# Optimization experiments

Measured on AMD Instinct MI355X. Metric: run time of the kernel, lower is better.

Reference implementation:

```python
import jax, jax.numpy as jnp
import numpy as np

DT = 0.001   # time step (s)
DX = 10.0    # grid spacing (m)


def setup_inputs() -> dict:
    key = jax.random.key(0)
    k1, k2, k3, k4, k5, k6 = jax.random.split(key, 6)
    B, H, W, NT, NR = 2, 256, 256, 600, 128
    # source wavelet per shot, [nt, batch]
    x = jax.random.normal(k1, (NT, B), dtype=jnp.float32)
    # velocity model in [1500, 4000] m/s -> Courant number vp*dt/dx <= 0.4 (stable)
    vp = 1500.0 + 2500.0 * jax.random.uniform(k2, (H, W), dtype=jnp.float32)
    src_y = jax.random.randint(k3, (B,), 8, H - 8)
    src_x = jax.random.randint(k4, (B,), 8, W - 8)
    rec_y = jax.random.randint(k5, (NR,), 8, H - 8)
    rec_x = jax.random.randint(k6, (NR,), 8, W - 8)
    return {"x": x, "vp": vp, "src_y": src_y, "src_x": src_x,
            "rec_y": rec_y, "rec_x": rec_x}


def _laplacian(u):
    # 5-point stencil with zero (Dirichlet) boundary, u: [B, H, W]
    up = jnp.pad(u, ((0, 0), (1, 1), (1, 1)))
    return (up[:, :-2, 1:-1] + up[:, 2:, 1:-1]
            + up[:, 1:-1, :-2] + up[:, 1:-1, 2:] - 4.0 * u)


def reference(x, vp, src_y, src_x, rec_y, rec_x):
    """Second-order acoustic FDTD: scan over time, per-step source scatter
    and receiver gather (the WaveRNN forward loop)."""
    NT, B = x.shape
    H, W = vp.shape
    c2 = (vp * (DT / DX)) ** 2          # [H, W] squared Courant number
    bidx = jnp.arange(B)

    def step(carry, xi):
        u1, u2 = carry                   # u_t, u_{t-1}: [B, H, W]
        u = 2.0 * u1 - u2 + c2[None] * _laplacian(u1)
        # source injection (smask scatter): one point source per shot
        u = u.at[bidx, src_y, src_x].add(xi)
        # probe recording (gather): shared receiver array across shots
        rec = u[:, rec_y, rec_x]         # [B, NR]
        return (u, u1), rec

    u0 = jnp.zeros((B, H, W), dtype=x.dtype)
    _, recs = jax.lax.scan(step, (u0, u0), x)
    return recs                           # [NT, B, NR]
```

## Files before the change

### kernel.cpp

```cpp
#include <hip/hip_runtime.h>
#include <hip/hip_cooperative_groups.h>

namespace cg = cooperative_groups;


#define HH 256
#define WW 256
#define KT 16
#define SHR 16
#define NSTRIP (HH / SHR)
#define NSLOT 16
#define RPT 3
#define NTH 1024
#define C2SCALE 1.0e-4f
#define NRMAX 128

__device__ __forceinline__ float dpp_west(float v) {
    return __int_as_float(__builtin_amdgcn_mov_dpp(__float_as_int(v), 0x138, 0xf, 0xf, true));
}
__device__ __forceinline__ float dpp_east(float v) {
    return __int_as_float(__builtin_amdgcn_mov_dpp(__float_as_int(v), 0x130, 0xf, 0xf, true));
}

#define ZERO4 make_float4(0.f, 0.f, 0.f, 0.f)

#define LAPROW(P, NN, CC, SS, CI)                                            \
    {                                                                        \
        const float wl_ = dpp_west((CC).w);                                  \
        const float er_ = dpp_east((CC).x);                                  \
        const float lx_ = (NN).x + (SS).x + wl_    + (CC).y - 4.0f * (CC).x; \
        const float ly_ = (NN).y + (SS).y + (CC).x + (CC).z - 4.0f * (CC).y; \
        const float lz_ = (NN).z + (SS).z + (CC).y + (CC).w - 4.0f * (CC).z; \
        const float lw_ = (NN).w + (SS).w + (CC).z + er_    - 4.0f * (CC).w; \
        (P).x = 2.0f * (CC).x - (P).x + (CI).x * lx_;                        \
        (P).y = 2.0f * (CC).y - (P).y + (CI).y * ly_;                        \
        (P).z = 2.0f * (CC).z - (P).z + (CI).z * lz_;                        \
        (P).w = 2.0f * (CC).w - (P).w + (CI).w * lw_;                        \
    }

#define INJECT(P) { if (sc == 0) (P).x += xi_; else if (sc == 1) (P).y += xi_; \
                    else if (sc == 2) (P).z += xi_; else (P).w += xi_; }

#define EMIT1(E, A0, A1, A2)                                                 \
    { const int pk_ = (E); const int rr_ = (pk_ >> 2) & 7; const int c_ = pk_ & 3; \
      const float4 uu_ = (rr_ == 0) ? (A0) : ((rr_ == 1) ? (A1) : (A2));     \
      const float v_ = (c_ == 0) ? uu_.x : ((c_ == 1) ? uu_.y : ((c_ == 2) ? uu_.z : uu_.w));  \
      obuf[sidx_][pk_ >> 5] = v_; }

#define STEP(U0, U1, U2, P0, P1, P2, BS, BD, SIDX)                           \
    {                                                                        \
        const int sidx_ = (SIDX);                                            \
        float4 nin_ = ZERO4, sin_ = ZERO4;                                   \
        if (!north_zero) nin_ = *(const float4*)&bnd[BS][rs - 1][1][xg];     \
        if (!south_zero) sin_ = *(const float4*)&bnd[BS][rs + 1][0][xg];     \
        LAPROW(P1, U0, U1, U2, c21);                                         \
        LAPROW(P0, nin_, U0, U1, c20);                                       \
        LAPROW(P2, U1, U2, sin_, c22);                                       \
        if (mine_src) {                                                      \
            const float xi_ = xs[sidx_];                                     \
            if (srr == 0)      INJECT(P0)                                    \
            else if (srr == 1) INJECT(P1)                                    \
            else               INJECT(P2)                                    \
        }                                                                    \
        *(float4*)&bnd[BD][rs][0][xg] = P0;                                  \
        *(float4*)&bnd[BD][rs][1][xg] = P2;                                  \
        if (cnt > 0) {                                                       \
            EMIT1(e0, P0, P1, P2);                                           \
            if (cnt > 1) { EMIT1(e1, P0, P1, P2);                            \
              if (cnt > 2) { EMIT1(e2, P0, P1, P2);                          \
                if (cnt > 3) { EMIT1(e3, P0, P1, P2);                        \
                  if (cnt > 4) { EMIT1(e4, P0, P1, P2);                      \
                    if (cnt > 5) { EMIT1(e5, P0, P1, P2); } } } } }          \
        }                                                                    \
    }

#define LOADC2(I, C)                                                         \
    {                                                                        \
        const int r_ = r0 + (I);                                             \
        if (r_ < RL) {                                                       \
            const int gy_ = lo + r_;                                         \
            const float4 v_ = *(const float4*)&vp[gy_ * WW + xg];            \
            (C).x = v_.x * C2SCALE; (C).y = v_.y * C2SCALE;                  \
            (C).z = v_.z * C2SCALE; (C).w = v_.w * C2SCALE;                  \
            (C).x *= (C).x; (C).y *= (C).y; (C).z *= (C).z; (C).w *= (C).w;  \
        } else { (C) = ZERO4; }                                              \
    }

#define SAVEROW(I, U, P)                                                     \
    {                                                                        \
        const int r_ = r0 + (I);                                             \
        const int gy_ = lo + r_;                                             \
        if (r_ < RL && gy_ >= y0 && gy_ < y0 + SHR) {                        \
            const size_t gi_ = bbase + (size_t)gy_ * WW + xg;                \
            *(float4*)&gcur[gi_]  = (U);                                     \
            *(float4*)&gprev[gi_] = (P);                                     \
        }                                                                    \
    }

#define RELOADROW(I, U, P)                                                   \
    {                                                                        \
        const int r_ = r0 + (I);                                             \
        const int gy_ = lo + r_;                                             \
        if (r_ < RL && (gy_ < y0 || gy_ >= y0 + SHR)) {                      \
            const size_t gi_ = bbase + (size_t)gy_ * WW + xg;                \
            (U) = *(const float4*)&gcur[gi_];                                \
            (P) = *(const float4*)&gprev[gi_];                               \
        }                                                                    \
    }

__global__ void __launch_bounds__(NTH) __attribute__((amdgpu_waves_per_eu(1, 4)))
wave_persist(const float* __restrict__ x, const float* __restrict__ vp,
             const int* __restrict__ src_y, const int* __restrict__ src_x,
             const int* __restrict__ rec_y, const int* __restrict__ rec_x,
             float* __restrict__ gcur, float* __restrict__ gprev,
             float* __restrict__ out, int NT, int B, int NR)
{
    cg::grid_group gg = cg::this_grid();

    __shared__ float bnd[2][NSLOT][2][WW];
    __shared__ float obuf[KT][NRMAX];
    __shared__ int   rec_s[NRMAX];
    __shared__ float xs[KT];

    const int strip = blockIdx.x;
    const int bb    = blockIdx.y;
    const int y0    = strip * SHR;
    const int lo    = max(0, y0 - KT);
    const int hi    = min(HH, y0 + SHR + KT);
    const int RL    = hi - lo;

    const int tid  = threadIdx.x;
    const int lane = tid & 63;
    const int rs   = tid >> 6;
    const int xg   = lane * 4;
    const int r0   = rs * RPT;
    const int gy0  = lo + r0;

    const size_t bbase = (size_t)bb * HH * WW;

    if (tid < NR) rec_s[tid] = (rec_y[tid] << 8) | rec_x[tid];

    float4 u0 = ZERO4, u1 = ZERO4, u2 = ZERO4;
    float4 p0 = ZERO4, p1 = ZERO4, p2 = ZERO4;
    float4 c20, c21, c22;
    LOADC2(0, c20); LOADC2(1, c21); LOADC2(2, c22);

    const int sy = src_y[bb];
    const int sx = src_x[bb];
    const int srr = sy - gy0;
    const bool mine_src = (sy >= lo) && (sy < hi) &&
                          (srr >= 0) && (srr < RPT) && ((sx >> 2) == lane);
    const int sc = sx & 3;

    __syncthreads();

    int e0 = 0, e1 = 0, e2 = 0, e3 = 0, e4 = 0, e5 = 0, cnt = 0;
    for (int k = 0; k < NR; ++k) {
        const int rc = rec_s[k];
        const int ry = rc >> 8;
        if (ry >= y0 && ry < y0 + SHR) {
            const int rr = ry - gy0;
            if (rr >= 0 && rr < RPT) {
                const int rx = rc & 255;
                if ((rx >> 2) == lane) {
                    const int pk = (k << 5) | (rr << 2) | (rx & 3);
                    if (cnt == 0) e0 = pk; else if (cnt == 1) e1 = pk;
                    else if (cnt == 2) e2 = pk; else if (cnt == 3) e3 = pk;
                    else if (cnt == 4) e4 = pk; else e5 = pk;
                    ++cnt;
                }
            }
        }
    }

    const bool north_zero = (rs == 0);
    const bool south_zero = (rs == NSLOT - 1) || (gy0 + RPT - 1 == HH - 1);

    for (int t0 = 0; t0 < NT; t0 += KT) {
        const int ns = (NT - t0 < KT) ? (NT - t0) : KT;

        if (tid < ns) xs[tid] = x[(t0 + tid) * B + bb];
        *(float4*)&bnd[0][rs][0][xg] = u0;
        *(float4*)&bnd[0][rs][1][xg] = u2;
        __syncthreads();

        #pragma unroll 1
        for (int s = 0; s < ns; s += 2) {
            STEP(u0, u1, u2, p0, p1, p2, 0, 1, s);
            __syncthreads();
            STEP(p0, p1, p2, u0, u1, u2, 1, 0, s + 1);
            __syncthreads();
        }

        for (int p = tid; p < KT * NRMAX; p += NTH) {
            const int s = p >> 7;
            const int k = p & 127;
            if (s < ns && k < NR) {
                const int rc = rec_s[k];
                const int ry = rc >> 8;
                if (ry >= y0 && ry < y0 + SHR) {
                    out[(size_t)(t0 + s) * B * NR + (size_t)bb * NR + k] = obuf[s][k];
                }
            }
        }

        if (t0 + KT < NT) {
            SAVEROW(0, u0, p0); SAVEROW(1, u1, p1); SAVEROW(2, u2, p2);
            gg.sync();
            RELOADROW(0, u0, p0); RELOADROW(1, u1, p1); RELOADROW(2, u2, p2);
        }
    }
}

extern "C" void kernel_launch(void* const* d_in, const int* in_sizes, int n_in,
                              void* d_out, int out_size, void* d_ws, size_t ws_size,
                              hipStream_t stream) {
    const float* x     = (const float*)d_in[0];
    const float* vp    = (const float*)d_in[1];
    const int* src_y   = (const int*)d_in[2];
    const int* src_x   = (const int*)d_in[3];
    const int* rec_y   = (const int*)d_in[4];
    const int* rec_x   = (const int*)d_in[5];

    int B  = in_sizes[2];
    int NR = in_sizes[4];
    int NT = in_sizes[0] / B;

    float* gcur  = (float*)d_ws;
    float* gprev = gcur + (size_t)B * HH * WW;
    float* outp  = (float*)d_out;

    void* args[] = { (void*)&x, (void*)&vp, (void*)&src_y, (void*)&src_x,
                     (void*)&rec_y, (void*)&rec_x, (void*)&gcur, (void*)&gprev,
                     (void*)&outp, (void*)&NT, (void*)&B, (void*)&NR };

    hipLaunchCooperativeKernel((const void*)wave_persist,
                               dim3(NSTRIP, B), dim3(NTH), args, 0, stream);
}
```

Measured before the change: 717.9 us.

## Replace grid-wide sync with neighbor flag handshakes and double-buffered halo exchange

Replaces the cooperative-groups grid barrier between time chunks with per-block release flags. Each strip block waits only for its north and south neighbours. The exchange buffers for the current and previous fields are double-buffered by chunk parity, so a fast block cannot overwrite data a slower neighbour is still reading. This removes the full-grid barrier cost and lets strips drift relative to each other. In exchange it adds spin-wait polling, a flag memset launch, and extra workspace use.

```diff
diff --git a/kernel.cpp b/kernel.cpp
--- a/kernel.cpp
+++ b/kernel.cpp
@@ -1,7 +1,5 @@
 #include <hip/hip_runtime.h>
 #include <hip/hip_cooperative_groups.h>
-
-namespace cg = cooperative_groups;
 
 
 #define HH 256
@@ -14,6 +12,7 @@
 #define NTH 1024
 #define C2SCALE 1.0e-4f
 #define NRMAX 128
+#define FPAD 32
 
 __device__ __forceinline__ float dpp_west(float v) {
     return __int_as_float(__builtin_amdgcn_mov_dpp(__float_as_int(v), 0x138, 0xf, 0xf, true));
@@ -86,25 +85,25 @@
         } else { (C) = ZERO4; }                                              \
     }
 
-#define SAVEROW(I, U, P)                                                     \
+#define SAVEROW(I, U, P, XC, XP)                                             \
     {                                                                        \
         const int r_ = r0 + (I);                                             \
         const int gy_ = lo + r_;                                             \
         if (r_ < RL && gy_ >= y0 && gy_ < y0 + SHR) {                        \
             const size_t gi_ = bbase + (size_t)gy_ * WW + xg;                \
-            *(float4*)&gcur[gi_]  = (U);                                     \
-            *(float4*)&gprev[gi_] = (P);                                     \
-        }                                                                    \
-    }
-
-#define RELOADROW(I, U, P)                                                   \
+            *(float4*)&(XC)[gi_] = (U);                                      \
+            *(float4*)&(XP)[gi_] = (P);                                      \
+        }                                                                    \
+    }
+
+#define RELOADROW(I, U, P, XC, XP)                                           \
     {                                                                        \
         const int r_ = r0 + (I);                                             \
         const int gy_ = lo + r_;                                             \
         if (r_ < RL && (gy_ < y0 || gy_ >= y0 + SHR)) {                      \
             const size_t gi_ = bbase + (size_t)gy_ * WW + xg;                \
-            (U) = *(const float4*)&gcur[gi_];                                \
-            (P) = *(const float4*)&gprev[gi_];                               \
+            (U) = *(const float4*)&(XC)[gi_];                                \
+            (P) = *(const float4*)&(XP)[gi_];                                \
         }                                                                    \
     }
 
@@ -112,11 +111,11 @@
 wave_persist(const float* __restrict__ x, const float* __restrict__ vp,
              const int* __restrict__ src_y, const int* __restrict__ src_x,
              const int* __restrict__ rec_y, const int* __restrict__ rec_x,
-             float* __restrict__ gcur, float* __restrict__ gprev,
+             float* __restrict__ xc0, float* __restrict__ xc1,
+             float* __restrict__ xp0, float* __restrict__ xp1,
+             unsigned int* __restrict__ flags,
              float* __restrict__ out, int NT, int B, int NR)
 {
-    cg::grid_group gg = cg::this_grid();
-
     __shared__ float bnd[2][NSLOT][2][WW];
     __shared__ float obuf[KT][NRMAX];
     __shared__ int   rec_s[NRMAX];
@@ -137,6 +136,7 @@
     const int gy0  = lo + r0;
 
     const size_t bbase = (size_t)bb * HH * WW;
+    const int fme = (bb * NSTRIP + strip) * FPAD;
 
     if (tid < NR) rec_s[tid] = (rec_y[tid] << 8) | rec_x[tid];
 
@@ -176,7 +176,8 @@
     const bool north_zero = (rs == 0);
     const bool south_zero = (rs == NSLOT - 1) || (gy0 + RPT - 1 == HH - 1);
 
-    for (int t0 = 0; t0 < NT; t0 += KT) {
+    int cidx = 0;
+    for (int t0 = 0; t0 < NT; t0 += KT, ++cidx) {
         const int ns = (NT - t0 < KT) ? (NT - t0) : KT;
 
         if (tid < ns) xs[tid] = x[(t0 + tid) * B + bb];
@@ -205,9 +206,32 @@
         }
 
         if (t0 + KT < NT) {
-            SAVEROW(0, u0, p0); SAVEROW(1, u1, p1); SAVEROW(2, u2, p2);
-            gg.sync();
-            RELOADROW(0, u0, p0); RELOADROW(1, u1, p1); RELOADROW(2, u2, p2);
+            float* xc = (cidx & 1) ? xc1 : xc0;
+            float* xp = (cidx & 1) ? xp1 : xp0;
+
+            SAVEROW(0, u0, p0, xc, xp);
+            SAVEROW(1, u1, p1, xc, xp);
+            SAVEROW(2, u2, p2, xc, xp);
+            __threadfence();
+            __syncthreads();
+            if (tid == 0) {
+                __hip_atomic_store(&flags[fme], (unsigned)(cidx + 1),
+                                   __ATOMIC_RELEASE, __HIP_MEMORY_SCOPE_AGENT);
+                const unsigned want = (unsigned)(cidx + 1);
+                if (strip > 0)
+                    while (__hip_atomic_load(&flags[fme - FPAD], __ATOMIC_RELAXED,
+                                             __HIP_MEMORY_SCOPE_AGENT) < want)
+                        __builtin_amdgcn_s_sleep(8);
+                if (strip < NSTRIP - 1)
+                    while (__hip_atomic_load(&flags[fme + FPAD], __ATOMIC_RELAXED,
+                                             __HIP_MEMORY_SCOPE_AGENT) < want)
+                        __builtin_amdgcn_s_sleep(8);
+            }
+            __syncthreads();
+            __threadfence();
+            RELOADROW(0, u0, p0, xc, xp);
+            RELOADROW(1, u1, p1, xc, xp);
+            RELOADROW(2, u2, p2, xc, xp);
         }
     }
 }
@@ -226,13 +250,22 @@
     int NR = in_sizes[4];
     int NT = in_sizes[0] / B;
 
-    float* gcur  = (float*)d_ws;
-    float* gprev = gcur + (size_t)B * HH * WW;
-    float* outp  = (float*)d_out;
+    const size_t fld = (size_t)B * HH * WW;
+    float* xc0 = (float*)d_ws;
+    float* xc1 = xc0 + fld;
+    float* xp0 = xc1 + fld;
+    float* xp1 = xp0 + fld;
+    unsigned int* flags = (unsigned int*)(xp1 + fld);
+    float* outp = (float*)d_out;
+
+    hipMemsetAsync(flags, 0, (size_t)B * NSTRIP * FPAD * sizeof(unsigned int),
+                   stream);
 
     void* args[] = { (void*)&x, (void*)&vp, (void*)&src_y, (void*)&src_x,
-                     (void*)&rec_y, (void*)&rec_x, (void*)&gcur, (void*)&gprev,
-                     (void*)&outp, (void*)&NT, (void*)&B, (void*)&NR };
+                     (void*)&rec_y, (void*)&rec_x,
+                     (void*)&xc0, (void*)&xc1, (void*)&xp0, (void*)&xp1,
+                     (void*)&flags, (void*)&outp, (void*)&NT, (void*)&B,
+                     (void*)&NR };
 
     hipLaunchCooperativeKernel((const void*)wave_persist,
                                dim3(NSTRIP, B), dim3(NTH), args, 0, stream);
```

New measurement: 1.318 ms. 1.84x slower.
